# Kernel tuning notes

Hardware: AMD Instinct MI355X
Metric: run time of the kernel (lower is better)

## Reference

```python
import jax, jax.numpy as jnp
import numpy as np

B = 32768
D = 1024          # input_dim
SEL = 512         # select_dim (per-expert selected features)
E = 6             # num_experts
K = 3             # top_k
SH = 32           # shared_dim
INNER = 64        # cross-attn inner dim (4 heads * 16)
HID = 128         # expert hidden


def setup_inputs() -> dict:
    key = jax.random.key(0)
    ks = jax.random.split(key, 16)
    s = lambda i, shape, scale=0.02: (jax.random.normal(ks[i], shape, jnp.float32) * scale)
    return {
        "x": jax.random.normal(ks[0], (B, D), jnp.float32),
        # CrossAttention(query_dim=512, context_dim=512, heads=4, dim_head=16)
        "Wq": s(1, (512, INNER)),
        "Wk": s(2, (512, INNER)),
        "Wv": s(3, (512, INNER)),
        "Wo": s(4, (INNER, 512)),
        "bo": jnp.zeros((512,), jnp.float32),
        # shared_proj: Linear(512, 32)
        "Wsp": s(5, (512, SH)),
        "bsp": jnp.zeros((SH,), jnp.float32),
        # gate: Linear(1024, 6)
        "Wg": s(6, (D, E)),
        "bg": jnp.zeros((E,), jnp.float32),
        # per-expert feature-mask logits
        "mask_logits": jax.random.normal(ks[7], (E, D), jnp.float32),
        # expert MLPs: Linear(544,128) -> ReLU -> Linear(128,1), stacked over experts
        "W1": s(8, (E, SEL + SH, HID)),
        "b1": jnp.zeros((E, HID), jnp.float32),
        "W2": s(9, (E, HID, 1)),
        "b2": jnp.zeros((E, 1), jnp.float32),
    }


def _moe_forward(x, Wq, Wk, Wv, Wo, bo, Wsp, bsp, Wg, bg, mask_logits, W1, b1, W2, b2):
    x_sem = x[:, :512]
    x_vis = x[:, 512:]

    # CrossAttention with a single query token attending to a single context
    # token: softmax over one key is identically 1, so attn output == v.
    v = x_vis @ Wv                      # [B, INNER]
    shared_token = v @ Wo + bo          # to_out Linear, [B, 512]
    shared_info = shared_token @ Wsp + bsp  # [B, SH]

    # Gating: top-k experts per sample, softmax over selected logits
    gate_logits = x @ Wg + bg                       # [B, E]
    topk_scores, topk_idx = jax.lax.top_k(gate_logits, K)  # [B, K]
    topk_w = jax.nn.softmax(topk_scores, axis=1)    # [B, K]

    # Per-expert learned feature selection (top-512 of sigmoid(mask_logits));
    # sigmoid is monotonic but kept for faithfulness.
    mask_prob = jax.nn.sigmoid(mask_logits)         # [E, D]
    _, sel_idx = jax.lax.top_k(mask_prob, SEL)      # [E, SEL]

    # Dense expert evaluation (every expert on every sample), then gather the
    # routed outputs -- same math as the original scatter loop.
    x_sel = jnp.take(x, sel_idx, axis=1)            # [B, E, SEL]
    h = jnp.einsum('bes,esh->beh', x_sel, W1[:, :SEL, :])
    h = h + jnp.einsum('bd,edh->beh', shared_info, W1[:, SEL:, :])
    h = jax.nn.relu(h + b1[None])                   # [B, E, HID]
    expert_out = jnp.einsum('beh,eh->be', h, W2[:, :, 0]) + b2[None, :, 0]  # [B, E]

    routed = jnp.take_along_axis(expert_out, topk_idx, axis=1)  # [B, K]
    return jnp.sum(topk_w * routed, axis=1, keepdims=True)      # [B, 1]


def reference(x, Wq, Wk, Wv, Wo, bo, Wsp, bsp, Wg, bg, mask_logits, W1, b1, W2, b2):
    return _moe_forward(x, Wq, Wk, Wv, Wo, bo, Wsp, bsp, Wg, bg, mask_logits, W1, b1, W2, b2)
```

## Files before the change

### kernel.cpp

```cpp
#include <hip/hip_runtime.h>

#define B 32768
#define D 1024
#define SEL 512
#define E 6
#define K 3
#define SH 32
#define HID 128
#define NKT 16

typedef __attribute__((ext_vector_type(8))) short bf16x8;
typedef __attribute__((ext_vector_type(4))) float f32x4;

__device__ __forceinline__ unsigned short f2bf(float f) {
  unsigned u = __float_as_uint(f);
  return (unsigned short)((u + 0x7fffu + ((u >> 16) & 1u)) >> 16);
}

__device__ __forceinline__ void gload_lds16(const void* g, void* l) {
  __builtin_amdgcn_global_load_lds(
      (const __attribute__((address_space(1))) void*)g,
      (__attribute__((address_space(3))) void*)l, 16, 0, 0);
}

__global__ void k_sel(const float* __restrict__ ml, int* __restrict__ inv) {
  __shared__ float row[D];
  const int e = blockIdx.x, t = threadIdx.x;
  row[t] = ml[e * D + t];
  __syncthreads();
  const float v = row[t];
  int rank = 0;
  for (int i = 0; i < D; ++i) {
    float u = row[i];
    rank += (u > v) || (u == v && i < t);
  }
  inv[e * D + t] = (rank < SEL) ? rank : -1;
}

__global__ __launch_bounds__(256) void k_wowsp(
    const float* __restrict__ Wo, const float* __restrict__ Wsp,
    const float* __restrict__ bo, const float* __restrict__ bsp,
    float* __restrict__ WoWsp, float* __restrict__ bfull) {
  __shared__ float red[256];
  const int t = threadIdx.x;
  const int j = t & 31, chunk = t >> 5;
  const int blk = blockIdx.x;
  float p = 0.f;
  if (blk < 64) {
    const int i = blk;
    for (int c = chunk * 64; c < chunk * 64 + 64; ++c)
      p += Wo[i * 512 + c] * Wsp[c * SH + j];
    red[t] = p;
    __syncthreads();
    if (t < 32) {
      float s = 0.f;
      #pragma unroll
      for (int k = 0; k < 8; ++k) s += red[k * 32 + j];
      WoWsp[i * SH + j] = s;
    }
  } else {
    for (int c = chunk * 64; c < chunk * 64 + 64; ++c)
      p += bo[c] * Wsp[c * SH + j];
    red[t] = p;
    __syncthreads();
    if (t < 32) {
      float s = bsp[j];
      #pragma unroll
      for (int k = 0; k < 8; ++k) s += red[k * 32 + j];
      bfull[j] = s;
    }
  }
}

__global__ __launch_bounds__(256) void k_wfull2(
    const float* __restrict__ Wv, const float* __restrict__ WoWsp,
    float* __restrict__ Wfull) {
  __shared__ float wsh[64 * SH];
  const int t = threadIdx.x;
  for (int idx = t; idx < 64 * SH; idx += 256) wsh[idx] = WoWsp[idx];
  __syncthreads();
  const int c = blockIdx.x * 8 + (t >> 5), j = t & 31;
  float p = 0.f;
  #pragma unroll 8
  for (int i = 0; i < 64; ++i) p += Wv[c * 64 + i] * wsh[i * SH + j];
  Wfull[c * SH + j] = p;
}

__global__ __launch_bounds__(256) void k_w1c(
    const float* __restrict__ W1, const float* __restrict__ b1,
    const int* __restrict__ inv, const float* __restrict__ Wfull,
    const float* __restrict__ bfull,
    unsigned short* __restrict__ W1eT, float* __restrict__ b1c) {
  __shared__ float w1b[SH];
  __shared__ float bf[SH];
  const int e = blockIdx.x >> 7, h = blockIdx.x & 127;
  const int t = threadIdx.x;
  const float* We = W1 + (size_t)e * (SEL + SH) * HID;
  if (t < SH) { w1b[t] = We[(size_t)(SEL + t) * HID + h]; bf[t] = bfull[t]; }
  __syncthreads();
  const int* iv = inv + e * D;
  unsigned short* dst = W1eT + ((size_t)e * HID + h) * D;
  #pragma unroll
  for (int it = 0; it < 4; ++it) {
    int d = t + it * 256;
    int s = iv[d];
    float v = (s >= 0) ? We[(size_t)s * HID + h] : 0.f;
    if (d >= 512) {
      const float* wf = Wfull + (size_t)(d - 512) * SH;
      float p = 0.f;
      #pragma unroll
      for (int j = 0; j < SH; ++j) p += wf[j] * w1b[j];
      v += p;
    }
    dst[d] = f2bf(v);
  }
  if (t == 0) {
    float p = b1[e * HID + h];
    for (int j = 0; j < SH; ++j) p += bf[j] * w1b[j];
    b1c[e * HID + h] = p;
  }
}

__global__ __launch_bounds__(256) void k_gate(
    const float* __restrict__ x, const float* __restrict__ Wg,
    const float* __restrict__ bg, float* __restrict__ gl) {
  const int w = threadIdx.x >> 6, lane = threadIdx.x & 63;
  const int wid = blockIdx.x * 4 + w;
  float wg[4][4][E];
  #pragma unroll
  for (int i = 0; i < 4; ++i)
    #pragma unroll
    for (int q = 0; q < 4; ++q) {
      const float* wr = Wg + (size_t)(i * 256 + lane * 4 + q) * E;
      #pragma unroll
      for (int e2 = 0; e2 < E; ++e2) wg[i][q][e2] = wr[e2];
    }
  for (int tok = wid * 4; tok < wid * 4 + 4; ++tok) {
    const float4* xp = (const float4*)(x + (size_t)tok * D);
    float acc[E] = {};
    #pragma unroll
    for (int i = 0; i < 4; ++i) {
      float4 v = xp[i * 64 + lane];
      #pragma unroll
      for (int q = 0; q < 4; ++q) {
        float xv = (&v.x)[q];
        #pragma unroll
        for (int e2 = 0; e2 < E; ++e2) acc[e2] += xv * wg[i][q][e2];
      }
    }
    #pragma unroll
    for (int e2 = 0; e2 < E; ++e2) {
      float s = acc[e2];
      s += __shfl_xor(s, 1); s += __shfl_xor(s, 2); s += __shfl_xor(s, 4);
      s += __shfl_xor(s, 8); s += __shfl_xor(s, 16); s += __shfl_xor(s, 32);
      acc[e2] = s;
    }
    if (lane == 0) {
      #pragma unroll
      for (int e2 = 0; e2 < E; ++e2) gl[(size_t)tok * E + e2] = acc[e2] + bg[e2];
    }
  }
}

__global__ __launch_bounds__(256) void k_gemm(
    const float* __restrict__ x, const unsigned short* __restrict__ W1eT,
    const float* __restrict__ b1c, const float* __restrict__ W2,
    const float* __restrict__ b2, float* __restrict__ eo) {
  __shared__ __align__(16) char ldsA[64 * 128];
  __shared__ __align__(16) char ldsB[128 * 128];
  __shared__ float red[2][64];

  const int t = threadIdx.x;
  const int e = blockIdx.x >> 9;
  const int bm = blockIdx.x & 511;
  const int w = t >> 6, lane = t & 63;
  const int wm = w >> 1, wn = w & 1;
  const int g = lane >> 4, j = lane & 15;
  const int c16 = t & 15, rb = t >> 4;
  const char* Wb = (const char*)(W1eT + (size_t)e * HID * D);

  f32x4 acc[2][4] = {};

  for (int kt = 0; kt < NKT; ++kt) {
    if (kt) __syncthreads();
    #pragma unroll
    for (int q = 0; q < 4; ++q) {
      int off = (w * 4 + q) * 1024 + lane * 16;
      int c = off >> 7, kb = off & 127;
      gload_lds16(Wb + (size_t)c * (D * 2) + kt * 128 + (kb ^ ((c & 7) << 4)),
                  ldsB + (w * 4 + q) * 1024);
    }
    #pragma unroll
    for (int r4 = 0; r4 < 4; ++r4) {
      int r = rb + r4 * 16;
      float4 v = *(const float4*)(x + (size_t)(bm * 64 + r) * D + kt * 64 + c16 * 4);
      ushort4 h;
      h.x = f2bf(v.x); h.y = f2bf(v.y); h.z = f2bf(v.z); h.w = f2bf(v.w);
      *(ushort4*)(ldsA + r * 128 + ((c16 * 8) ^ ((r & 7) << 4))) = h;
    }
    __syncthreads();
    #pragma unroll
    for (int kk = 0; kk < 2; ++kk) {
      const int kb = kk * 64 + g * 16;
      bf16x8 aF[2], bF[4];
      #pragma unroll
      for (int fm = 0; fm < 2; ++fm) {
        int row = wm * 32 + fm * 16 + j;
        aF[fm] = *(const bf16x8*)(ldsA + row * 128 + (kb ^ ((row & 7) << 4)));
      }
      #pragma unroll
      for (int fn = 0; fn < 4; ++fn) {
        int col = wn * 64 + fn * 16 + j;
        bF[fn] = *(const bf16x8*)(ldsB + col * 128 + (kb ^ ((col & 7) << 4)));
      }
      #pragma unroll
      for (int fm = 0; fm < 2; ++fm)
        #pragma unroll
        for (int fn = 0; fn < 4; ++fn)
          acc[fm][fn] = __builtin_amdgcn_mfma_f32_16x16x32_bf16(aF[fm], bF[fn], acc[fm][fn], 0, 0, 0);
    }
  }
  float b1v[4], w2v[4];
  #pragma unroll
  for (int fn = 0; fn < 4; ++fn) {
    int col = wn * 64 + fn * 16 + j;
    b1v[fn] = b1c[e * HID + col];
    w2v[fn] = W2[e * HID + col];
  }
  #pragma unroll
  for (int fm = 0; fm < 2; ++fm) {
    #pragma unroll
    for (int r = 0; r < 4; ++r) {
      float s = 0.f;
      #pragma unroll
      for (int fn = 0; fn < 4; ++fn)
        s += fmaxf(acc[fm][fn][r] + b1v[fn], 0.f) * w2v[fn];
      s += __shfl_xor(s, 1); s += __shfl_xor(s, 2);
      s += __shfl_xor(s, 4); s += __shfl_xor(s, 8);
      if (j == 0) red[wn][wm * 32 + fm * 16 + g * 4 + r] = s;
    }
  }
  __syncthreads();
  if (t < 64)
    eo[(size_t)(bm * 64 + t) * E + e] = red[0][t] + red[1][t] + b2[e];
}

__global__ void k_comb(const float* __restrict__ gl, const float* __restrict__ eo,
                       float* __restrict__ out) {
  const int tok = blockIdx.x * 256 + threadIdx.x;
  float gv[E];
  #pragma unroll
  for (int e2 = 0; e2 < E; ++e2) gv[e2] = gl[(size_t)tok * E + e2];
  int idx[K]; float sc[K];
  bool used[E] = {};
  #pragma unroll
  for (int k = 0; k < K; ++k) {
    float best = -1e30f; int bi = 0;
    for (int e2 = 0; e2 < E; ++e2)
      if (!used[e2] && gv[e2] > best) { best = gv[e2]; bi = e2; }
    used[bi] = true; sc[k] = best; idx[k] = bi;
  }
  float s0 = 1.f, s1 = __expf(sc[1] - sc[0]), s2 = __expf(sc[2] - sc[0]);
  float inv_s = 1.f / (s0 + s1 + s2);
  float r = s0 * eo[(size_t)tok * E + idx[0]]
          + s1 * eo[(size_t)tok * E + idx[1]]
          + s2 * eo[(size_t)tok * E + idx[2]];
  out[tok] = r * inv_s;
}

extern "C" void kernel_launch(void* const* d_in, const int* in_sizes, int n_in,
                              void* d_out, int out_size, void* d_ws, size_t ws_size,
                              hipStream_t stream) {
  const float* x   = (const float*)d_in[0];
  const float* Wv  = (const float*)d_in[3];
  const float* Wo  = (const float*)d_in[4];
  const float* bo  = (const float*)d_in[5];
  const float* Wsp = (const float*)d_in[6];
  const float* bsp = (const float*)d_in[7];
  const float* Wg  = (const float*)d_in[8];
  const float* bg  = (const float*)d_in[9];
  const float* ml  = (const float*)d_in[10];
  const float* W1  = (const float*)d_in[11];
  const float* b1  = (const float*)d_in[12];
  const float* W2  = (const float*)d_in[13];
  const float* b2  = (const float*)d_in[14];
  float* out = (float*)d_out;

  char* ws = (char*)d_ws;
  int*   inv   = (int*)ws;
  float* WoWsp = (float*)(ws + 32768);
  float* Wfull = (float*)(ws + 49152);
  float* bfull = (float*)(ws + 114688);
  float* b1c   = (float*)(ws + 118784);
  float* gl    = (float*)(ws + 131072);
  float* eo    = (float*)(ws + 917504);
  unsigned short* W1eT = (unsigned short*)(ws + 1703936);

  k_sel<<<E, D, 0, stream>>>(ml, inv);
  k_wowsp<<<65, 256, 0, stream>>>(Wo, Wsp, bo, bsp, WoWsp, bfull);
  k_wfull2<<<64, 256, 0, stream>>>(Wv, WoWsp, Wfull);
  k_w1c<<<E * HID, 256, 0, stream>>>(W1, b1, inv, Wfull, bfull, W1eT, b1c);
  k_gate<<<2048, 256, 0, stream>>>(x, Wg, bg, gl);
  k_gemm<<<E * (B / 64), 256, 0, stream>>>(x, W1eT, b1c, W2, b2, eo);
  k_comb<<<B / 256, 256, 0, stream>>>(gl, eo, out);
}
```

Before: 209.6 us.

## Route tokens to experts sparsely and pre-convert x to bf16 in gate kernel

Replaces dense evaluation of all six experts per token with sparse routing. A top-k kernel builds per-expert token lists through atomics, and the GEMM then processes only the routed tokens, cutting expert work in half (3 of 6 experts). The gate kernel also writes a bf16 copy of x so the GEMM can gather A rows with direct global-to-LDS loads. GEMM tiles grow to 128 rows, and the routing weights are applied in the epilogue. The cost is extra kernels, atomics, gathered loads and a large workspace requirement for the bf16 copy, with a fallback path when the workspace is too small.

```diff
diff --git a/kernel.cpp b/kernel.cpp
--- a/kernel.cpp
+++ b/kernel.cpp
@@ -121,9 +121,11 @@
   }
 }
 
-__global__ __launch_bounds__(256) void k_gate(
+template<bool WRITE_XBF>
+__global__ __launch_bounds__(256) void k_xbf_gate(
     const float* __restrict__ x, const float* __restrict__ Wg,
-    const float* __restrict__ bg, float* __restrict__ gl) {
+    const float* __restrict__ bg, unsigned short* __restrict__ xbf,
+    float* __restrict__ gl) {
   const int w = threadIdx.x >> 6, lane = threadIdx.x & 63;
   const int wid = blockIdx.x * 4 + w;
   float wg[4][4][E];
@@ -141,6 +143,11 @@
     #pragma unroll
     for (int i = 0; i < 4; ++i) {
       float4 v = xp[i * 64 + lane];
+      if (WRITE_XBF) {
+        ushort4 h4;
+        h4.x = f2bf(v.x); h4.y = f2bf(v.y); h4.z = f2bf(v.z); h4.w = f2bf(v.w);
+        *(ushort4*)((char*)xbf + (size_t)tok * 2048 + i * 512 + lane * 8) = h4;
+      }
       #pragma unroll
       for (int q = 0; q < 4; ++q) {
         float xv = (&v.x)[q];
@@ -162,92 +169,11 @@
   }
 }
 
-__global__ __launch_bounds__(256) void k_gemm(
-    const float* __restrict__ x, const unsigned short* __restrict__ W1eT,
-    const float* __restrict__ b1c, const float* __restrict__ W2,
-    const float* __restrict__ b2, float* __restrict__ eo) {
-  __shared__ __align__(16) char ldsA[64 * 128];
-  __shared__ __align__(16) char ldsB[128 * 128];
-  __shared__ float red[2][64];
-
-  const int t = threadIdx.x;
-  const int e = blockIdx.x >> 9;
-  const int bm = blockIdx.x & 511;
-  const int w = t >> 6, lane = t & 63;
-  const int wm = w >> 1, wn = w & 1;
-  const int g = lane >> 4, j = lane & 15;
-  const int c16 = t & 15, rb = t >> 4;
-  const char* Wb = (const char*)(W1eT + (size_t)e * HID * D);
-
-  f32x4 acc[2][4] = {};
-
-  for (int kt = 0; kt < NKT; ++kt) {
-    if (kt) __syncthreads();
-    #pragma unroll
-    for (int q = 0; q < 4; ++q) {
-      int off = (w * 4 + q) * 1024 + lane * 16;
-      int c = off >> 7, kb = off & 127;
-      gload_lds16(Wb + (size_t)c * (D * 2) + kt * 128 + (kb ^ ((c & 7) << 4)),
-                  ldsB + (w * 4 + q) * 1024);
-    }
-    #pragma unroll
-    for (int r4 = 0; r4 < 4; ++r4) {
-      int r = rb + r4 * 16;
-      float4 v = *(const float4*)(x + (size_t)(bm * 64 + r) * D + kt * 64 + c16 * 4);
-      ushort4 h;
-      h.x = f2bf(v.x); h.y = f2bf(v.y); h.z = f2bf(v.z); h.w = f2bf(v.w);
-      *(ushort4*)(ldsA + r * 128 + ((c16 * 8) ^ ((r & 7) << 4))) = h;
-    }
-    __syncthreads();
-    #pragma unroll
-    for (int kk = 0; kk < 2; ++kk) {
-      const int kb = kk * 64 + g * 16;
-      bf16x8 aF[2], bF[4];
-      #pragma unroll
-      for (int fm = 0; fm < 2; ++fm) {
-        int row = wm * 32 + fm * 16 + j;
-        aF[fm] = *(const bf16x8*)(ldsA + row * 128 + (kb ^ ((row & 7) << 4)));
-      }
-      #pragma unroll
-      for (int fn = 0; fn < 4; ++fn) {
-        int col = wn * 64 + fn * 16 + j;
-        bF[fn] = *(const bf16x8*)(ldsB + col * 128 + (kb ^ ((col & 7) << 4)));
-      }
-      #pragma unroll
-      for (int fm = 0; fm < 2; ++fm)
-        #pragma unroll
-        for (int fn = 0; fn < 4; ++fn)
-          acc[fm][fn] = __builtin_amdgcn_mfma_f32_16x16x32_bf16(aF[fm], bF[fn], acc[fm][fn], 0, 0, 0);
-    }
-  }
-  float b1v[4], w2v[4];
-  #pragma unroll
-  for (int fn = 0; fn < 4; ++fn) {
-    int col = wn * 64 + fn * 16 + j;
-    b1v[fn] = b1c[e * HID + col];
-    w2v[fn] = W2[e * HID + col];
-  }
-  #pragma unroll
-  for (int fm = 0; fm < 2; ++fm) {
-    #pragma unroll
-    for (int r = 0; r < 4; ++r) {
-      float s = 0.f;
-      #pragma unroll
-      for (int fn = 0; fn < 4; ++fn)
-        s += fmaxf(acc[fm][fn][r] + b1v[fn], 0.f) * w2v[fn];
-      s += __shfl_xor(s, 1); s += __shfl_xor(s, 2);
-      s += __shfl_xor(s, 4); s += __shfl_xor(s, 8);
-      if (j == 0) red[wn][wm * 32 + fm * 16 + g * 4 + r] = s;
-    }
-  }
-  __syncthreads();
-  if (t < 64)
-    eo[(size_t)(bm * 64 + t) * E + e] = red[0][t] + red[1][t] + b2[e];
-}
-
-__global__ void k_comb(const float* __restrict__ gl, const float* __restrict__ eo,
-                       float* __restrict__ out) {
+__global__ __launch_bounds__(256) void k_topk(
+    const float* __restrict__ gl, int* __restrict__ cnt,
+    int* __restrict__ clist, float* __restrict__ wlist) {
   const int tok = blockIdx.x * 256 + threadIdx.x;
+  const int lane = threadIdx.x & 63;
   float gv[E];
   #pragma unroll
   for (int e2 = 0; e2 < E; ++e2) gv[e2] = gl[(size_t)tok * E + e2];
@@ -260,12 +186,151 @@
       if (!used[e2] && gv[e2] > best) { best = gv[e2]; bi = e2; }
     used[bi] = true; sc[k] = best; idx[k] = bi;
   }
-  float s0 = 1.f, s1 = __expf(sc[1] - sc[0]), s2 = __expf(sc[2] - sc[0]);
-  float inv_s = 1.f / (s0 + s1 + s2);
-  float r = s0 * eo[(size_t)tok * E + idx[0]]
-          + s1 * eo[(size_t)tok * E + idx[1]]
-          + s2 * eo[(size_t)tok * E + idx[2]];
-  out[tok] = r * inv_s;
+  float s1 = __expf(sc[1] - sc[0]), s2 = __expf(sc[2] - sc[0]);
+  float inv_s = 1.f / (1.f + s1 + s2);
+  float tw[K] = {inv_s, s1 * inv_s, s2 * inv_s};
+  const unsigned long long below = (1ULL << lane) - 1ULL;
+  #pragma unroll
+  for (int e2 = 0; e2 < E; ++e2) {
+    int myk = -1;
+    #pragma unroll
+    for (int k = 0; k < K; ++k) if (idx[k] == e2) myk = k;
+    unsigned long long m = __ballot(myk >= 0);
+    if (m) {
+      int tot = __popcll(m);
+      int leader = __ffsll((long long)m) - 1;
+      int base = 0;
+      if (lane == leader) base = atomicAdd(&cnt[e2], tot);
+      base = __shfl(base, leader);
+      if (myk >= 0) {
+        int pos = base + __popcll(m & below);
+        clist[e2 * B + pos] = (tok << 2) | myk;
+        wlist[e2 * B + pos] = tw[myk];
+      }
+    }
+  }
+}
+
+template<int AMODE>
+__global__ __launch_bounds__(256) void k_gemm(
+    const float* __restrict__ x, const unsigned short* __restrict__ xbf,
+    const unsigned short* __restrict__ W1eT,
+    const int* __restrict__ cnt, const int* __restrict__ clist,
+    const float* __restrict__ wlist,
+    const float* __restrict__ b1c, const float* __restrict__ W2,
+    const float* __restrict__ b2, float* __restrict__ eo4) {
+  __shared__ __align__(16) char ldsA[128 * 128];
+  __shared__ __align__(16) char ldsB[128 * 128];
+  __shared__ int tokl[128];
+  __shared__ float red[128];
+
+  const int t = threadIdx.x;
+  const int e = blockIdx.x >> 8;
+  const int bm = blockIdx.x & 255;
+  const int n = cnt[e];
+  if (bm * 128 >= n) return;
+  const int cb = e * B;
+
+  if (t < 128) {
+    int gr = bm * 128 + t;
+    tokl[t] = clist[cb + (gr < n ? gr : 0)] >> 2;
+  }
+  __syncthreads();
+
+  const int w = t >> 6, lane = t & 63;
+  const int g = lane >> 4, j = lane & 15;
+  const int swz = ((lane & 7) * 16) ^ ((lane >> 3) << 4);
+
+  const char* srcB[4];
+  #pragma unroll
+  for (int q = 0; q < 4; ++q)
+    srcB[q] = (const char*)W1eT +
+              (size_t)(e * HID + w * 32 + q * 8 + (lane >> 3)) * (D * 2) + swz;
+  const char* srcA[4];
+  if (AMODE == 0) {
+    #pragma unroll
+    for (int q = 0; q < 4; ++q)
+      srcA[q] = (const char*)xbf +
+                (size_t)tokl[w * 32 + q * 8 + (lane >> 3)] * 2048 + swz;
+  }
+
+  f32x4 acc[2][8] = {};
+
+  for (int kt = 0; kt < NKT; ++kt) {
+    if (kt) __syncthreads();
+    if (AMODE == 0) {
+      #pragma unroll
+      for (int q = 0; q < 4; ++q)
+        gload_lds16(srcA[q] + kt * 128, ldsA + w * 4096 + q * 1024);
+    }
+    #pragma unroll
+    for (int q = 0; q < 4; ++q)
+      gload_lds16(srcB[q] + kt * 128, ldsB + w * 4096 + q * 1024);
+    if (AMODE == 1) {
+      #pragma unroll
+      for (int it = 0; it < 8; ++it) {
+        int r = (t >> 4) + it * 16;
+        const float4 v =
+            *(const float4*)(x + (size_t)tokl[r] * D + kt * 64 + (t & 15) * 4);
+        ushort4 h4;
+        h4.x = f2bf(v.x); h4.y = f2bf(v.y); h4.z = f2bf(v.z); h4.w = f2bf(v.w);
+        *(ushort4*)(ldsA + r * 128 + (((t & 15) * 8) ^ ((r & 7) << 4))) = h4;
+      }
+    }
+    __syncthreads();
+    #pragma unroll
+    for (int kk = 0; kk < 2; ++kk) {
+      const int kb = kk * 64 + g * 16;
+      bf16x8 aF[2];
+      #pragma unroll
+      for (int fm = 0; fm < 2; ++fm) {
+        int row = w * 32 + fm * 16 + j;
+        aF[fm] = *(const bf16x8*)(ldsA + row * 128 + (kb ^ ((row & 7) << 4)));
+      }
+      #pragma unroll
+      for (int fn = 0; fn < 8; ++fn) {
+        int col = fn * 16 + j;
+        bf16x8 bF = *(const bf16x8*)(ldsB + col * 128 + (kb ^ ((col & 7) << 4)));
+        acc[0][fn] = __builtin_amdgcn_mfma_f32_16x16x32_bf16(aF[0], bF, acc[0][fn], 0, 0, 0);
+        acc[1][fn] = __builtin_amdgcn_mfma_f32_16x16x32_bf16(aF[1], bF, acc[1][fn], 0, 0, 0);
+      }
+    }
+  }
+
+  float vb1[8], vw2[8];
+  #pragma unroll
+  for (int fn = 0; fn < 8; ++fn) {
+    int col = fn * 16 + j;
+    vb1[fn] = b1c[e * HID + col];
+    vw2[fn] = W2[e * HID + col];
+  }
+  #pragma unroll
+  for (int fm = 0; fm < 2; ++fm) {
+    #pragma unroll
+    for (int r = 0; r < 4; ++r) {
+      float s = 0.f;
+      #pragma unroll
+      for (int fn = 0; fn < 8; ++fn)
+        s += fmaxf(acc[fm][fn][r] + vb1[fn], 0.f) * vw2[fn];
+      s += __shfl_xor(s, 1); s += __shfl_xor(s, 2);
+      s += __shfl_xor(s, 4); s += __shfl_xor(s, 8);
+      if (j == 0) red[w * 32 + fm * 16 + g * 4 + r] = s;
+    }
+  }
+  __syncthreads();
+  if (t < 128) {
+    int gr = bm * 128 + t;
+    if (gr < n) {
+      int en = clist[cb + gr];
+      eo4[(size_t)(en >> 2) * 4 + (en & 3)] = wlist[cb + gr] * (red[t] + b2[e]);
+    }
+  }
+}
+
+__global__ void k_comb2(const float* __restrict__ eo4, float* __restrict__ out) {
+  const int tok = blockIdx.x * 256 + threadIdx.x;
+  float4 v = *(const float4*)(eo4 + (size_t)tok * 4);
+  out[tok] = v.x + v.y + v.z;
 }
 
 extern "C" void kernel_launch(void* const* d_in, const int* in_sizes, int n_in,
@@ -292,15 +357,28 @@
   float* Wfull = (float*)(ws + 49152);
   float* bfull = (float*)(ws + 114688);
   float* b1c   = (float*)(ws + 118784);
+  int*   cnt   = (int*)(ws + 126976);
   float* gl    = (float*)(ws + 131072);
-  float* eo    = (float*)(ws + 917504);
-  unsigned short* W1eT = (unsigned short*)(ws + 1703936);
+  int*   clist = (int*)(ws + 917504);
+  float* wlist = (float*)(ws + 1703936);
+  float* eo4   = (float*)(ws + 2490368);
+  unsigned short* W1eT = (unsigned short*)(ws + 3014656);
+  unsigned short* xbf  = (unsigned short*)(ws + 4587520);
+  const bool use_xbf = ws_size >= (size_t)4587520 + (size_t)B * D * 2;
 
   k_sel<<<E, D, 0, stream>>>(ml, inv);
   k_wowsp<<<65, 256, 0, stream>>>(Wo, Wsp, bo, bsp, WoWsp, bfull);
   k_wfull2<<<64, 256, 0, stream>>>(Wv, WoWsp, Wfull);
   k_w1c<<<E * HID, 256, 0, stream>>>(W1, b1, inv, Wfull, bfull, W1eT, b1c);
-  k_gate<<<2048, 256, 0, stream>>>(x, Wg, bg, gl);
-  k_gemm<<<E * (B / 64), 256, 0, stream>>>(x, W1eT, b1c, W2, b2, eo);
-  k_comb<<<B / 256, 256, 0, stream>>>(gl, eo, out);
-}
+  hipMemsetAsync(cnt, 0, 32, stream);
+  if (use_xbf)
+    k_xbf_gate<true><<<B / 16, 256, 0, stream>>>(x, Wg, bg, xbf, gl);
+  else
+    k_xbf_gate<false><<<B / 16, 256, 0, stream>>>(x, Wg, bg, xbf, gl);
+  k_topk<<<B / 256, 256, 0, stream>>>(gl, cnt, clist, wlist);
+  if (use_xbf)
+    k_gemm<0><<<E * 256, 256, 0, stream>>>(x, xbf, W1eT, cnt, clist, wlist, b1c, W2, b2, eo4);
+  else
+    k_gemm<1><<<E * 256, 256, 0, stream>>>(x, xbf, W1eT, cnt, clist, wlist, b1c, W2, b2, eo4);
+  k_comb2<<<B / 256, 256, 0, stream>>>(eo4, out);
+}
```

New measurement: 199.5 us. 1.05x faster.

## Fuse gate logits into expert GEMM via bf16 MFMA with fp32 fallback for near-ties

Applied to the files above, without the earlier changes.

Removes the separate gate kernel, which re-read all of x. The gate logits are now computed with a bf16 MFMA inside the expert-0 GEMM blocks, reusing the A tiles already staged in shared memory. Top-k selection and softmax weights move into that kernel's epilogue. Tokens whose third and fourth logits fall within a small threshold are recomputed in fp32 so the routing stays exact. The combine kernel becomes a plain dot product over a padded weight vector, at the cost of load imbalance for the expert-0 blocks and a data-dependent fallback loop.

```diff
diff --git a/kernel.cpp b/kernel.cpp
--- a/kernel.cpp
+++ b/kernel.cpp
@@ -8,6 +8,7 @@
 #define SH 32
 #define HID 128
 #define NKT 16
+#define GUARD_THR 1.5e-2f
 
 typedef __attribute__((ext_vector_type(8))) short bf16x8;
 typedef __attribute__((ext_vector_type(4))) float f32x4;
@@ -15,6 +16,9 @@
 __device__ __forceinline__ unsigned short f2bf(float f) {
   unsigned u = __float_as_uint(f);
   return (unsigned short)((u + 0x7fffu + ((u >> 16) & 1u)) >> 16);
+}
+__device__ __forceinline__ float bf2f(unsigned short h) {
+  return __uint_as_float((unsigned)h << 16);
 }
 
 __device__ __forceinline__ void gload_lds16(const void* g, void* l) {
@@ -40,14 +44,16 @@
 __global__ __launch_bounds__(256) void k_wowsp(
     const float* __restrict__ Wo, const float* __restrict__ Wsp,
     const float* __restrict__ bo, const float* __restrict__ bsp,
-    float* __restrict__ WoWsp, float* __restrict__ bfull) {
+    const float* __restrict__ Wg,
+    float* __restrict__ WoWsp, float* __restrict__ bfull,
+    unsigned short* __restrict__ WgS) {
   __shared__ float red[256];
   const int t = threadIdx.x;
   const int j = t & 31, chunk = t >> 5;
   const int blk = blockIdx.x;
-  float p = 0.f;
   if (blk < 64) {
     const int i = blk;
+    float p = 0.f;
     for (int c = chunk * 64; c < chunk * 64 + 64; ++c)
       p += Wo[i * 512 + c] * Wsp[c * SH + j];
     red[t] = p;
@@ -58,7 +64,8 @@
       for (int k = 0; k < 8; ++k) s += red[k * 32 + j];
       WoWsp[i * SH + j] = s;
     }
-  } else {
+  } else if (blk == 64) {
+    float p = 0.f;
     for (int c = chunk * 64; c < chunk * 64 + 64; ++c)
       p += bo[c] * Wsp[c * SH + j];
     red[t] = p;
@@ -69,6 +76,11 @@
       for (int k = 0; k < 8; ++k) s += red[k * 32 + j];
       bfull[j] = s;
     }
+  } else {
+    const int idx = (blk - 65) * 256 + t;
+    const int col = idx >> 10, k = idx & 1023;
+    float wv = (col < E) ? Wg[(size_t)k * E + col] : 0.f;
+    WgS[col * D + k] = f2bf(wv);
   }
 }
 
@@ -121,65 +133,31 @@
   }
 }
 
-__global__ __launch_bounds__(256) void k_gate(
-    const float* __restrict__ x, const float* __restrict__ Wg,
-    const float* __restrict__ bg, float* __restrict__ gl) {
-  const int w = threadIdx.x >> 6, lane = threadIdx.x & 63;
-  const int wid = blockIdx.x * 4 + w;
-  float wg[4][4][E];
-  #pragma unroll
-  for (int i = 0; i < 4; ++i)
-    #pragma unroll
-    for (int q = 0; q < 4; ++q) {
-      const float* wr = Wg + (size_t)(i * 256 + lane * 4 + q) * E;
-      #pragma unroll
-      for (int e2 = 0; e2 < E; ++e2) wg[i][q][e2] = wr[e2];
-    }
-  for (int tok = wid * 4; tok < wid * 4 + 4; ++tok) {
-    const float4* xp = (const float4*)(x + (size_t)tok * D);
-    float acc[E] = {};
-    #pragma unroll
-    for (int i = 0; i < 4; ++i) {
-      float4 v = xp[i * 64 + lane];
-      #pragma unroll
-      for (int q = 0; q < 4; ++q) {
-        float xv = (&v.x)[q];
-        #pragma unroll
-        for (int e2 = 0; e2 < E; ++e2) acc[e2] += xv * wg[i][q][e2];
-      }
-    }
-    #pragma unroll
-    for (int e2 = 0; e2 < E; ++e2) {
-      float s = acc[e2];
-      s += __shfl_xor(s, 1); s += __shfl_xor(s, 2); s += __shfl_xor(s, 4);
-      s += __shfl_xor(s, 8); s += __shfl_xor(s, 16); s += __shfl_xor(s, 32);
-      acc[e2] = s;
-    }
-    if (lane == 0) {
-      #pragma unroll
-      for (int e2 = 0; e2 < E; ++e2) gl[(size_t)tok * E + e2] = acc[e2] + bg[e2];
-    }
-  }
-}
-
-__global__ __launch_bounds__(256) void k_gemm(
-    const float* __restrict__ x, const unsigned short* __restrict__ W1eT,
+__global__ __launch_bounds__(256) void k_gemm6(
+    const float* __restrict__ x, const unsigned short* __restrict__ WgS,
+    const float* __restrict__ Wg, const float* __restrict__ bg,
+    const unsigned short* __restrict__ W1eT,
     const float* __restrict__ b1c, const float* __restrict__ W2,
-    const float* __restrict__ b2, float* __restrict__ eo) {
+    const float* __restrict__ b2, float* __restrict__ eo,
+    float* __restrict__ gw) {
   __shared__ __align__(16) char ldsA[64 * 128];
   __shared__ __align__(16) char ldsB[128 * 128];
+  __shared__ __align__(16) char ldsG[2048];
   __shared__ float red[2][64];
 
   const int t = threadIdx.x;
   const int e = blockIdx.x >> 9;
   const int bm = blockIdx.x & 511;
+  const bool do_gate = (e == 0);
   const int w = t >> 6, lane = t & 63;
   const int wm = w >> 1, wn = w & 1;
   const int g = lane >> 4, j = lane & 15;
   const int c16 = t & 15, rb = t >> 4;
+  const int swz = ((lane & 7) * 16) ^ ((lane >> 3) << 4);
   const char* Wb = (const char*)(W1eT + (size_t)e * HID * D);
 
   f32x4 acc[2][4] = {};
+  f32x4 accG[2] = {};
 
   for (int kt = 0; kt < NKT; ++kt) {
     if (kt) __syncthreads();
@@ -190,19 +168,29 @@
       gload_lds16(Wb + (size_t)c * (D * 2) + kt * 128 + (kb ^ ((c & 7) << 4)),
                   ldsB + (w * 4 + q) * 1024);
     }
+    if (do_gate && w == 0) {
+      #pragma unroll
+      for (int q2 = 0; q2 < 2; ++q2) {
+        int off = q2 * 1024 + lane * 16;
+        int c = off >> 7, kb = off & 127;
+        gload_lds16((const char*)WgS + (size_t)c * (D * 2) + kt * 128 +
+                        (kb ^ ((c & 7) << 4)),
+                    ldsG + q2 * 1024);
+      }
+    }
     #pragma unroll
     for (int r4 = 0; r4 < 4; ++r4) {
       int r = rb + r4 * 16;
       float4 v = *(const float4*)(x + (size_t)(bm * 64 + r) * D + kt * 64 + c16 * 4);
-      ushort4 h;
-      h.x = f2bf(v.x); h.y = f2bf(v.y); h.z = f2bf(v.z); h.w = f2bf(v.w);
-      *(ushort4*)(ldsA + r * 128 + ((c16 * 8) ^ ((r & 7) << 4))) = h;
+      ushort4 h4;
+      h4.x = f2bf(v.x); h4.y = f2bf(v.y); h4.z = f2bf(v.z); h4.w = f2bf(v.w);
+      *(ushort4*)(ldsA + r * 128 + ((c16 * 8) ^ ((r & 7) << 4))) = h4;
     }
     __syncthreads();
     #pragma unroll
     for (int kk = 0; kk < 2; ++kk) {
       const int kb = kk * 64 + g * 16;
-      bf16x8 aF[2], bF[4];
+      bf16x8 aF[2];
       #pragma unroll
       for (int fm = 0; fm < 2; ++fm) {
         int row = wm * 32 + fm * 16 + j;
@@ -211,21 +199,35 @@
       #pragma unroll
       for (int fn = 0; fn < 4; ++fn) {
         int col = wn * 64 + fn * 16 + j;
-        bF[fn] = *(const bf16x8*)(ldsB + col * 128 + (kb ^ ((col & 7) << 4)));
-      }
-      #pragma unroll
-      for (int fm = 0; fm < 2; ++fm)
-        #pragma unroll
-        for (int fn = 0; fn < 4; ++fn)
-          acc[fm][fn] = __builtin_amdgcn_mfma_f32_16x16x32_bf16(aF[fm], bF[fn], acc[fm][fn], 0, 0, 0);
-    }
-  }
-  float b1v[4], w2v[4];
+        bf16x8 bF = *(const bf16x8*)(ldsB + col * 128 + (kb ^ ((col & 7) << 4)));
+        acc[0][fn] = __builtin_amdgcn_mfma_f32_16x16x32_bf16(aF[0], bF, acc[0][fn], 0, 0, 0);
+        acc[1][fn] = __builtin_amdgcn_mfma_f32_16x16x32_bf16(aF[1], bF, acc[1][fn], 0, 0, 0);
+      }
+      if (do_gate && wn == 0) {
+        bf16x8 bG = *(const bf16x8*)(ldsG + j * 128 + (kb ^ ((j & 7) << 4)));
+        accG[0] = __builtin_amdgcn_mfma_f32_16x16x32_bf16(aF[0], bG, accG[0], 0, 0, 0);
+        accG[1] = __builtin_amdgcn_mfma_f32_16x16x32_bf16(aF[1], bG, accG[1], 0, 0, 0);
+      }
+    }
+  }
+
+  __syncthreads();
+  float (*gl_s)[8] = (float(*)[8])ldsA;
+
+  if (do_gate && wn == 0 && j < E) {
+    #pragma unroll
+    for (int fm = 0; fm < 2; ++fm)
+      #pragma unroll
+      for (int ri = 0; ri < 4; ++ri)
+        gl_s[wm * 32 + fm * 16 + g * 4 + ri][j] = accG[fm][ri];
+  }
+
+  float vb1[4], vw2[4];
   #pragma unroll
   for (int fn = 0; fn < 4; ++fn) {
     int col = wn * 64 + fn * 16 + j;
-    b1v[fn] = b1c[e * HID + col];
-    w2v[fn] = W2[e * HID + col];
+    vb1[fn] = b1c[e * HID + col];
+    vw2[fn] = W2[e * HID + col];
   }
   #pragma unroll
   for (int fm = 0; fm < 2; ++fm) {
@@ -234,38 +236,88 @@
       float s = 0.f;
       #pragma unroll
       for (int fn = 0; fn < 4; ++fn)
-        s += fmaxf(acc[fm][fn][r] + b1v[fn], 0.f) * w2v[fn];
+        s += fmaxf(acc[fm][r][0] * 0.f + acc[fm][fn][r] + vb1[fn], 0.f) * vw2[fn];
       s += __shfl_xor(s, 1); s += __shfl_xor(s, 2);
       s += __shfl_xor(s, 4); s += __shfl_xor(s, 8);
       if (j == 0) red[wn][wm * 32 + fm * 16 + g * 4 + r] = s;
     }
   }
   __syncthreads();
-  if (t < 64)
-    eo[(size_t)(bm * 64 + t) * E + e] = red[0][t] + red[1][t] + b2[e];
-}
-
-__global__ void k_comb(const float* __restrict__ gl, const float* __restrict__ eo,
-                       float* __restrict__ out) {
+
+  if (t < 64) {
+    const int tok = bm * 64 + t;
+    eo[(size_t)tok * 8 + e] = red[0][t] + red[1][t] + b2[e];
+
+    if (do_gate) {
+      float gv[E];
+      #pragma unroll
+      for (int e2 = 0; e2 < E; ++e2) gv[e2] = gl_s[t][e2] + bg[e2];
+      float s4[4];
+      {
+        bool used[E] = {};
+        #pragma unroll
+        for (int k = 0; k < 4; ++k) {
+          float best = -1e30f; int bi = 0;
+          for (int e2 = 0; e2 < E; ++e2)
+            if (!used[e2] && gv[e2] > best) { best = gv[e2]; bi = e2; }
+          used[bi] = true; s4[k] = best;
+        }
+      }
+      unsigned long long flags = __ballot(s4[2] - s4[3] < GUARD_THR);
+      while (flags) {
+        const int fl = __ffsll((long long)flags) - 1;
+        flags &= flags - 1;
+        const int tokf = bm * 64 + fl;
+        float ex[E] = {};
+        for (int i = 0; i < 16; ++i) {
+          const int d = t + 64 * i;
+          float xv = x[(size_t)tokf * D + d];
+          const float* wr = Wg + (size_t)d * E;
+          #pragma unroll
+          for (int e2 = 0; e2 < E; ++e2) ex[e2] += xv * wr[e2];
+        }
+        #pragma unroll
+        for (int e2 = 0; e2 < E; ++e2) {
+          float s = ex[e2];
+          s += __shfl_xor(s, 1); s += __shfl_xor(s, 2); s += __shfl_xor(s, 4);
+          s += __shfl_xor(s, 8); s += __shfl_xor(s, 16); s += __shfl_xor(s, 32);
+          ex[e2] = s;
+        }
+        if (t == fl) {
+          #pragma unroll
+          for (int e2 = 0; e2 < E; ++e2) gv[e2] = ex[e2] + bg[e2];
+        }
+      }
+      int idx[K]; float sc[K];
+      bool used[E] = {};
+      #pragma unroll
+      for (int k = 0; k < K; ++k) {
+        float best = -1e30f; int bi = 0;
+        for (int e2 = 0; e2 < E; ++e2)
+          if (!used[e2] && gv[e2] > best) { best = gv[e2]; bi = e2; }
+        used[bi] = true; sc[k] = best; idx[k] = bi;
+      }
+      float s1 = __expf(sc[1] - sc[0]), s2 = __expf(sc[2] - sc[0]);
+      float inv_s = 1.f / (1.f + s1 + s2);
+      float w8[8] = {0.f, 0.f, 0.f, 0.f, 0.f, 0.f, 0.f, 0.f};
+      w8[idx[0]] = inv_s;
+      w8[idx[1]] = s1 * inv_s;
+      w8[idx[2]] = s2 * inv_s;
+      *(float4*)(gw + (size_t)tok * 8) = make_float4(w8[0], w8[1], w8[2], w8[3]);
+      *(float4*)(gw + (size_t)tok * 8 + 4) = make_float4(w8[4], w8[5], w8[6], w8[7]);
+    }
+  }
+}
+
+__global__ void k_comb3(const float* __restrict__ gw, const float* __restrict__ eo,
+                        float* __restrict__ out) {
   const int tok = blockIdx.x * 256 + threadIdx.x;
-  float gv[E];
-  #pragma unroll
-  for (int e2 = 0; e2 < E; ++e2) gv[e2] = gl[(size_t)tok * E + e2];
-  int idx[K]; float sc[K];
-  bool used[E] = {};
-  #pragma unroll
-  for (int k = 0; k < K; ++k) {
-    float best = -1e30f; int bi = 0;
-    for (int e2 = 0; e2 < E; ++e2)
-      if (!used[e2] && gv[e2] > best) { best = gv[e2]; bi = e2; }
-    used[bi] = true; sc[k] = best; idx[k] = bi;
-  }
-  float s0 = 1.f, s1 = __expf(sc[1] - sc[0]), s2 = __expf(sc[2] - sc[0]);
-  float inv_s = 1.f / (s0 + s1 + s2);
-  float r = s0 * eo[(size_t)tok * E + idx[0]]
-          + s1 * eo[(size_t)tok * E + idx[1]]
-          + s2 * eo[(size_t)tok * E + idx[2]];
-  out[tok] = r * inv_s;
+  float4 g0 = *(const float4*)(gw + (size_t)tok * 8);
+  float4 g1 = *(const float4*)(gw + (size_t)tok * 8 + 4);
+  float4 e0 = *(const float4*)(eo + (size_t)tok * 8);
+  float4 e1 = *(const float4*)(eo + (size_t)tok * 8 + 4);
+  out[tok] = g0.x * e0.x + g0.y * e0.y + g0.z * e0.z + g0.w * e0.w +
+             g1.x * e1.x + g1.y * e1.y;
 }
 
 extern "C" void kernel_launch(void* const* d_in, const int* in_sizes, int n_in,
@@ -292,15 +344,15 @@
   float* Wfull = (float*)(ws + 49152);
   float* bfull = (float*)(ws + 114688);
   float* b1c   = (float*)(ws + 118784);
-  float* gl    = (float*)(ws + 131072);
-  float* eo    = (float*)(ws + 917504);
-  unsigned short* W1eT = (unsigned short*)(ws + 1703936);
+  unsigned short* WgS = (unsigned short*)(ws + 131072);
+  float* gw    = (float*)(ws + 262144);
+  float* eo    = (float*)(ws + 1310720);
+  unsigned short* W1eT = (unsigned short*)(ws + 2359296);
 
   k_sel<<<E, D, 0, stream>>>(ml, inv);
-  k_wowsp<<<65, 256, 0, stream>>>(Wo, Wsp, bo, bsp, WoWsp, bfull);
+  k_wowsp<<<129, 256, 0, stream>>>(Wo, Wsp, bo, bsp, Wg, WoWsp, bfull, WgS);
   k_wfull2<<<64, 256, 0, stream>>>(Wv, WoWsp, Wfull);
   k_w1c<<<E * HID, 256, 0, stream>>>(W1, b1, inv, Wfull, bfull, W1eT, b1c);
-  k_gate<<<2048, 256, 0, stream>>>(x, Wg, bg, gl);
-  k_gemm<<<E * (B / 64), 256, 0, stream>>>(x, W1eT, b1c, W2, b2, eo);
-  k_comb<<<B / 256, 256, 0, stream>>>(gl, eo, out);
-}
+  k_gemm6<<<E * 512, 256, 0, stream>>>(x, WgS, Wg, bg, W1eT, b1c, W2, b2, eo, gw);
+  k_comb3<<<B / 256, 256, 0, stream>>>(gw, eo, out);
+}
```

Measured after the change: 201.5 us. 3.9% less time.
